# Optimization experiments

Measured on AMD Instinct MI355X. Metric: run time of the kernel, lower is better.

The kernel has to match this reference:

```python
import jax, jax.numpy as jnp
import numpy as np

N_MESH = 40962
N_GRID = 262144
N_EDGE = 786432
D = 128       # node/edge feature dim
H = 256       # MLP hidden dim
EPS = 1e-5


def _layernorm(x, g, b):
    m = jnp.mean(x, axis=-1, keepdims=True)
    v = jnp.mean(jnp.square(x - m), axis=-1, keepdims=True)
    return (x - m) * jax.lax.rsqrt(v + EPS) * g + b


def _mlp(x, W1, b1, W2, b2, g, beta):
    # Linear -> SiLU -> Linear -> LayerNorm (hidden_layers=1)
    h = jax.nn.silu(x @ W1 + b1)
    return _layernorm(h @ W2 + b2, g, beta)


def setup_inputs() -> dict:
    key = jax.random.key(0)
    ks = jax.random.split(key, 20)
    s = 0.02
    inp = {
        "m2g_efeat": jax.random.normal(ks[0], (N_EDGE, D), jnp.float32),
        "grid_nfeat": jax.random.normal(ks[1], (N_GRID, D), jnp.float32),
        "mesh_nfeat": jax.random.normal(ks[2], (N_MESH, D), jnp.float32),
        "src_idx": jax.random.randint(ks[3], (N_EDGE,), 0, N_MESH, jnp.int32),
        "dst_idx": jax.random.randint(ks[4], (N_EDGE,), 0, N_GRID, jnp.int32),
        # edge MLP: concat(efeat, src, dst) [3D] -> H -> D, LayerNorm
        "eW1": jax.random.normal(ks[5], (3 * D, H), jnp.float32) * s,
        "eb1": jnp.zeros((H,), jnp.float32),
        "eW2": jax.random.normal(ks[6], (H, D), jnp.float32) * s,
        "eb2": jnp.zeros((D,), jnp.float32),
        "eg": jnp.ones((D,), jnp.float32),
        "ebeta": jnp.zeros((D,), jnp.float32),
        # node MLP: concat(agg_efeat, grid_nfeat) [2D] -> H -> D, LayerNorm
        "nW1": jax.random.normal(ks[7], (2 * D, H), jnp.float32) * s,
        "nb1": jnp.zeros((H,), jnp.float32),
        "nW2": jax.random.normal(ks[8], (H, D), jnp.float32) * s,
        "nb2": jnp.zeros((D,), jnp.float32),
        "ng": jnp.ones((D,), jnp.float32),
        "nbeta": jnp.zeros((D,), jnp.float32),
    }
    return inp


def reference(m2g_efeat, grid_nfeat, mesh_nfeat, src_idx, dst_idx,
              eW1, eb1, eW2, eb2, eg, ebeta,
              nW1, nb1, nW2, nb2, ng, nbeta):
    # --- edge MLP (MeshGraphEdgeMLPConcat): gather src/dst, concat, MLP ---
    cat_e = jnp.concatenate(
        [m2g_efeat, mesh_nfeat[src_idx], grid_nfeat[dst_idx]], axis=-1)  # [E, 3D]
    efeat = _mlp(cat_e, eW1, eb1, eW2, eb2, eg, ebeta)                   # [E, D]
    # --- aggregate_and_concat: scatter-sum to dst nodes, concat dst feats ---
    agg = jax.ops.segment_sum(efeat, dst_idx, num_segments=N_GRID)       # [N_grid, D]
    cat_n = jnp.concatenate([agg, grid_nfeat], axis=-1)                  # [N_grid, 2D]
    # --- node MLP + residual ---
    return _mlp(cat_n, nW1, nb1, nW2, nb2, ng, nbeta) + grid_nfeat
```

## Files before the change

### kernel.cpp

```cpp
#include <hip/hip_runtime.h>
#include <hip/hip_bf16.h>

typedef __bf16 bf16_t;
typedef bf16_t bf16x8 __attribute__((ext_vector_type(8)));
typedef float f32x16 __attribute__((ext_vector_type(16)));

#define MFMA32(a, b, c) __builtin_amdgcn_mfma_f32_32x32x16_bf16(a, b, c, 0, 0, 0)

static constexpr int E_EDGE = 786432;
static constexpr int N_GRID = 262144;

static constexpr int E_LDT = 136;
static constexpr int E_ATB = 64 * E_LDT * 2;
static constexpr int E_LDH = 264;
static constexpr int E_LDO = 132;
static constexpr int E_OFF_IDX = 2 * E_ATB;
static constexpr int E_SMEM = E_OFF_IDX + 3 * 256;

__device__ __forceinline__ void lds_barrier() {
    asm volatile("s_waitcnt lgkmcnt(0)" ::: "memory");
    __builtin_amdgcn_s_barrier();
    __builtin_amdgcn_sched_barrier(0);
}

__device__ __forceinline__ float fast_silu(float x) {
    return x * __builtin_amdgcn_rcpf(1.f + __expf(-x));
}

__global__ void pack_w1(const float* __restrict__ w, bf16_t* __restrict__ out, int tsteps) {
    const int gid = blockIdx.x * 256 + threadIdx.x;
    if (gid >= tsteps * 8 * 8 * 64) return;
    const int lane = gid & 63, grp = gid >> 6;
    const int wave = grp & 7, ks = (grp >> 3) & 7, t = grp >> 6;
    const int n = wave * 32 + (lane & 31);
    const int kb = t * 128 + ks * 16 + (lane >> 5) * 8;
    union { bf16_t h[8]; uint4 u; } pk;
#pragma unroll
    for (int j = 0; j < 8; ++j) pk.h[j] = (bf16_t)w[(size_t)(kb + j) * 256 + n];
    reinterpret_cast<uint4*>(out)[gid] = pk.u;
}

__global__ void pack_w2(const float* __restrict__ w, bf16_t* __restrict__ out) {
    const int gid = blockIdx.x * 256 + threadIdx.x;
    if (gid >= 16 * 4 * 64) return;
    const int lane = gid & 63, grp = gid >> 6;
    const int wn = grp & 3, ks = grp >> 2;
    const int n = wn * 32 + (lane & 31);
    const int kb = ks * 16 + (lane >> 5) * 8;
    union { bf16_t h[8]; uint4 u; } pk;
#pragma unroll
    for (int j = 0; j < 8; ++j) pk.h[j] = (bf16_t)w[(size_t)(kb + j) * 128 + n];
    reinterpret_cast<uint4*>(out)[gid] = pk.u;
}

__global__ void f32_to_bf16_vec(const float* __restrict__ in, bf16_t* __restrict__ out, int n8) {
    int i = blockIdx.x * 256 + threadIdx.x;
    if (i < n8) {
        const float4* p = reinterpret_cast<const float4*>(in + (size_t)i * 8);
        const float4 a = p[0], b = p[1];
        union { bf16_t h[8]; uint4 u; } pk;
        pk.h[0] = (bf16_t)a.x; pk.h[1] = (bf16_t)a.y; pk.h[2] = (bf16_t)a.z; pk.h[3] = (bf16_t)a.w;
        pk.h[4] = (bf16_t)b.x; pk.h[5] = (bf16_t)b.y; pk.h[6] = (bf16_t)b.z; pk.h[7] = (bf16_t)b.w;
        reinterpret_cast<uint4*>(out)[i] = pk.u;
    }
}

__global__ void k_hist(const int* __restrict__ dst, int* __restrict__ deg, int E) {
    int i = blockIdx.x * 256 + threadIdx.x;
    if (i < E) atomicAdd(&deg[dst[i]], 1);
}

__global__ void k_scan1(const int* __restrict__ deg, int* __restrict__ excl,
                        int* __restrict__ bsum) {
    __shared__ int sd[256];
    const int b = blockIdx.x, t = threadIdx.x;
    int4 v = reinterpret_cast<const int4*>(deg)[b * 256 + t];
    const int s0 = v.x, s1 = s0 + v.y, s2 = s1 + v.z, s3 = s2 + v.w;
    sd[t] = s3;
    __syncthreads();
    for (int off = 1; off < 256; off <<= 1) {
        int val = (t >= off) ? sd[t - off] : 0;
        __syncthreads();
        if (t >= off) sd[t] += val;
        __syncthreads();
    }
    const int pre = (t > 0) ? sd[t - 1] : 0;
    int4 o;
    o.x = pre; o.y = pre + s0; o.z = pre + s1; o.w = pre + s2;
    reinterpret_cast<int4*>(excl)[b * 256 + t] = o;
    if (t == 255) bsum[b] = sd[255];
}

__global__ void k_scan2(const int* __restrict__ bsum, int* __restrict__ bofs) {
    __shared__ int sd[256];
    const int t = threadIdx.x;
    sd[t] = bsum[t];
    __syncthreads();
    for (int off = 1; off < 256; off <<= 1) {
        int val = (t >= off) ? sd[t - off] : 0;
        __syncthreads();
        if (t >= off) sd[t] += val;
        __syncthreads();
    }
    bofs[t] = (t > 0) ? sd[t - 1] : 0;
}

__global__ void k_scan3(const int* __restrict__ excl, const int* __restrict__ bofs,
                        int* __restrict__ rowptr, int* __restrict__ cursor, int N, int E) {
    int i = blockIdx.x * 256 + threadIdx.x;
    if (i < N) {
        const int v = excl[i] + bofs[i >> 10];
        rowptr[i] = v;
        cursor[i] = v;
    }
    if (i == 0) rowptr[N] = E;
}

__global__ void k_slot(const int* __restrict__ dst, int* __restrict__ cursor,
                       int* __restrict__ slot, int E) {
    int i = blockIdx.x * 256 + threadIdx.x;
    if (i < E) slot[i] = atomicAdd(&cursor[dst[i]], 1);
}

__global__ __launch_bounds__(512, 8) void edge_mlp(
    const float* __restrict__ m2g,
    const bf16_t* __restrict__ gridb, const bf16_t* __restrict__ meshb,
    const int* __restrict__ src_idx, const int* __restrict__ dst_idx,
    const int* __restrict__ slot,
    const bf16_t* __restrict__ W1P,
    const float* __restrict__ b1,
    const bf16_t* __restrict__ W2P,
    const float* __restrict__ b2,
    const float* __restrict__ g, const float* __restrict__ beta,
    bf16_t* __restrict__ efs) {
    __shared__ __align__(16) char smem[E_SMEM];

    const int tid = threadIdx.x;
    const int wave = tid >> 6, lane = tid & 63;
    const int l31 = lane & 31, lk = lane >> 5;
    const int wm = wave >> 2, wn = wave & 3;
    const int r0 = blockIdx.x * 64;
    const int srow = tid >> 3, sc = (tid & 7) * 16;

    int* sidx = (int*)(smem + E_OFF_IDX);
    int* didx = sidx + 64;
    int* slotl = didx + 64;
    if (tid < 64) sidx[tid] = src_idx[r0 + tid];
    else if (tid < 128) didx[tid - 64] = dst_idx[r0 + tid - 64];
    else if (tid < 192) slotl[tid - 128] = slot[r0 + tid - 128];
    lds_barrier();

    bf16_t* buf0 = (bf16_t*)smem;
    bf16_t* buf1 = (bf16_t*)(smem + E_ATB);

    {
        float4 f0[4];
        const float* p0 = m2g + (size_t)(r0 + srow) * 128 + sc;
#pragma unroll
        for (int j = 0; j < 4; ++j) f0[j] = *reinterpret_cast<const float4*>(p0 + j * 4);
        bf16_t* dst = buf0 + srow * E_LDT + sc;
#pragma unroll
        for (int q = 0; q < 2; ++q) {
            union { bf16_t h[8]; uint4 u; } pk;
            const float4 v0 = f0[q * 2], v1 = f0[q * 2 + 1];
            pk.h[0] = (bf16_t)v0.x; pk.h[1] = (bf16_t)v0.y;
            pk.h[2] = (bf16_t)v0.z; pk.h[3] = (bf16_t)v0.w;
            pk.h[4] = (bf16_t)v1.x; pk.h[5] = (bf16_t)v1.y;
            pk.h[6] = (bf16_t)v1.z; pk.h[7] = (bf16_t)v1.w;
            *reinterpret_cast<uint4*>(dst + q * 8) = pk.u;
        }
    }
    uint4 a1[2];
    {
        const bf16_t* p1 = meshb + (size_t)sidx[srow] * 128 + sc;
        a1[0] = *reinterpret_cast<const uint4*>(p1);
        a1[1] = *reinterpret_cast<const uint4*>(p1 + 8);
    }
    lds_barrier();

    f32x16 acc[2] = {};
    auto COMPUTE = [&](const bf16_t* A, int t) {
#pragma unroll
        for (int ks = 0; ks < 8; ++ks) {
            const bf16x8 bw = *reinterpret_cast<const bf16x8*>(
                W1P + ((size_t)((t * 8 + ks) * 8 + wave) * 64 + lane) * 8);
            const int kb = ks * 16 + lk * 8;
            bf16x8 a[2];
#pragma unroll
            for (int mt = 0; mt < 2; ++mt)
                a[mt] = *reinterpret_cast<const bf16x8*>(A + (mt * 32 + l31) * E_LDT + kb);
#pragma unroll
            for (int mt = 0; mt < 2; ++mt)
                acc[mt] = MFMA32(a[mt], bw, acc[mt]);
        }
    };

    uint4 a2[2];
    {
        const bf16_t* p2 = gridb + (size_t)didx[srow] * 128 + sc;
        a2[0] = *reinterpret_cast<const uint4*>(p2);
        a2[1] = *reinterpret_cast<const uint4*>(p2 + 8);
    }
    {
        bf16_t* dst = buf1 + srow * E_LDT + sc;
        *reinterpret_cast<uint4*>(dst) = a1[0];
        *reinterpret_cast<uint4*>(dst + 8) = a1[1];
    }
    COMPUTE(buf0, 0);
    lds_barrier();
    {
        bf16_t* dst = buf0 + srow * E_LDT + sc;
        *reinterpret_cast<uint4*>(dst) = a2[0];
        *reinterpret_cast<uint4*>(dst + 8) = a2[1];
    }
    COMPUTE(buf1, 1);
    lds_barrier();
    COMPUTE(buf0, 2);
    lds_barrier();

    bf16_t* hT = (bf16_t*)smem;
    {
        const int col = wave * 32 + l31;
        const float bb = b1[col];
#pragma unroll
        for (int mt = 0; mt < 2; ++mt)
#pragma unroll
            for (int r = 0; r < 16; ++r) {
                const int row = mt * 32 + (r & 3) + 8 * (r >> 2) + 4 * lk;
                hT[row * E_LDH + col] = (bf16_t)fast_silu(acc[mt][r] + bb);
            }
    }
    lds_barrier();

    f32x16 acc2 = {};
#pragma unroll
    for (int ks = 0; ks < 16; ++ks) {
        const bf16x8 bw = *reinterpret_cast<const bf16x8*>(
            W2P + ((size_t)(ks * 4 + wn) * 64 + lane) * 8);
        const int kb = ks * 16 + lk * 8;
        const bf16x8 a = *reinterpret_cast<const bf16x8*>(hT + (wm * 32 + l31) * E_LDH + kb);
        acc2 = MFMA32(a, bw, acc2);
    }
    lds_barrier();

    float* outl = (float*)smem;
    {
        const int col = wn * 32 + l31;
        const float bb = b2[col];
#pragma unroll
        for (int r = 0; r < 16; ++r) {
            const int row = wm * 32 + (r & 3) + 8 * (r >> 2) + 4 * lk;
            outl[row * E_LDO + col] = acc2[r] + bb;
        }
    }
    lds_barrier();

    {
        const int lrow = tid >> 3, lq = (tid & 7) * 16;
        const float* rpd = outl + lrow * E_LDO + lq;
        float s = 0.f, sq2 = 0.f;
#pragma unroll
        for (int q = 0; q < 4; ++q) {
            const float4 v = *reinterpret_cast<const float4*>(rpd + q * 4);
            s += v.x + v.y + v.z + v.w;
            sq2 += v.x * v.x + v.y * v.y + v.z * v.z + v.w * v.w;
        }
        s += __shfl_xor(s, 1);  sq2 += __shfl_xor(sq2, 1);
        s += __shfl_xor(s, 2);  sq2 += __shfl_xor(sq2, 2);
        s += __shfl_xor(s, 4);  sq2 += __shfl_xor(sq2, 4);
        const float mean = s * (1.f / 128.f);
        const float var = sq2 * (1.f / 128.f) - mean * mean;
        const float rstd = rsqrtf(var + 1e-5f);

        const int sl = slotl[lrow];
        bf16_t* op = efs + (size_t)sl * 128 + lq;
        union { bf16_t h[16]; uint4 u[2]; } pk;
#pragma unroll
        for (int q = 0; q < 4; ++q) {
            const float4 v = *reinterpret_cast<const float4*>(rpd + q * 4);
            const float4 gv = *reinterpret_cast<const float4*>(g + lq + q * 4);
            const float4 bv = *reinterpret_cast<const float4*>(beta + lq + q * 4);
            pk.h[q * 4 + 0] = (bf16_t)((v.x - mean) * rstd * gv.x + bv.x);
            pk.h[q * 4 + 1] = (bf16_t)((v.y - mean) * rstd * gv.y + bv.y);
            pk.h[q * 4 + 2] = (bf16_t)((v.z - mean) * rstd * gv.z + bv.z);
            pk.h[q * 4 + 3] = (bf16_t)((v.w - mean) * rstd * gv.w + bv.w);
        }
        *reinterpret_cast<uint4*>(op) = pk.u[0];
        *reinterpret_cast<uint4*>(op + 8) = pk.u[1];
    }
}

__global__ __launch_bounds__(512, 8) void node_mlp(
    const bf16_t* __restrict__ efs,
    const int* __restrict__ rowptr,
    const bf16_t* __restrict__ gridb,
    const float* __restrict__ gridf,
    const bf16_t* __restrict__ W1P,
    const float* __restrict__ b1,
    const bf16_t* __restrict__ W2P,
    const float* __restrict__ b2,
    const float* __restrict__ g, const float* __restrict__ beta,
    float* __restrict__ outp) {
    __shared__ __align__(16) char smem[E_SMEM];

    const int tid = threadIdx.x;
    const int wave = tid >> 6, lane = tid & 63;
    const int l31 = lane & 31, lk = lane >> 5;
    const int wm = wave >> 2, wn = wave & 3;
    const int r0 = blockIdx.x * 64;
    const int srow = tid >> 3, sc = (tid & 7) * 16;

    bf16_t* buf0 = (bf16_t*)smem;
    bf16_t* buf1 = (bf16_t*)(smem + E_ATB);
    int* rp = (int*)(smem + E_OFF_IDX);

    if (tid < 65) rp[tid] = rowptr[r0 + tid];
    lds_barrier();

    {
        const int beg = rp[srow], end = rp[srow + 1];
        float s[16];
#pragma unroll
        for (int i = 0; i < 16; ++i) s[i] = 0.f;
        for (int e = beg; e < end; ++e) {
            const bf16_t* p = efs + (size_t)e * 128 + sc;
            bf16x8 v0 = *reinterpret_cast<const bf16x8*>(p);
            bf16x8 v1 = *reinterpret_cast<const bf16x8*>(p + 8);
#pragma unroll
            for (int i = 0; i < 8; ++i) {
                s[i] += (float)v0[i];
                s[8 + i] += (float)v1[i];
            }
        }
        union { bf16_t h[16]; uint4 u[2]; } pk;
#pragma unroll
        for (int i = 0; i < 16; ++i) pk.h[i] = (bf16_t)s[i];
        bf16_t* dst = buf0 + srow * E_LDT + sc;
        *reinterpret_cast<uint4*>(dst) = pk.u[0];
        *reinterpret_cast<uint4*>(dst + 8) = pk.u[1];
    }
    uint4 a1[2];
    {
        const bf16_t* p1 = gridb + (size_t)(r0 + srow) * 128 + sc;
        a1[0] = *reinterpret_cast<const uint4*>(p1);
        a1[1] = *reinterpret_cast<const uint4*>(p1 + 8);
    }
    lds_barrier();

    f32x16 acc[2] = {};
    auto COMPUTE = [&](const bf16_t* A, int t) {
#pragma unroll
        for (int ks = 0; ks < 8; ++ks) {
            const bf16x8 bw = *reinterpret_cast<const bf16x8*>(
                W1P + ((size_t)((t * 8 + ks) * 8 + wave) * 64 + lane) * 8);
            const int kb = ks * 16 + lk * 8;
            bf16x8 a[2];
#pragma unroll
            for (int mt = 0; mt < 2; ++mt)
                a[mt] = *reinterpret_cast<const bf16x8*>(A + (mt * 32 + l31) * E_LDT + kb);
#pragma unroll
            for (int mt = 0; mt < 2; ++mt)
                acc[mt] = MFMA32(a[mt], bw, acc[mt]);
        }
    };

    {
        bf16_t* dst = buf1 + srow * E_LDT + sc;
        *reinterpret_cast<uint4*>(dst) = a1[0];
        *reinterpret_cast<uint4*>(dst + 8) = a1[1];
    }
    COMPUTE(buf0, 0);
    lds_barrier();
    COMPUTE(buf1, 1);
    lds_barrier();

    bf16_t* hT = (bf16_t*)smem;
    {
        const int col = wave * 32 + l31;
        const float bb = b1[col];
#pragma unroll
        for (int mt = 0; mt < 2; ++mt)
#pragma unroll
            for (int r = 0; r < 16; ++r) {
                const int row = mt * 32 + (r & 3) + 8 * (r >> 2) + 4 * lk;
                hT[row * E_LDH + col] = (bf16_t)fast_silu(acc[mt][r] + bb);
            }
    }
    lds_barrier();

    f32x16 acc2 = {};
#pragma unroll
    for (int ks = 0; ks < 16; ++ks) {
        const bf16x8 bw = *reinterpret_cast<const bf16x8*>(
            W2P + ((size_t)(ks * 4 + wn) * 64 + lane) * 8);
        const int kb = ks * 16 + lk * 8;
        const bf16x8 a = *reinterpret_cast<const bf16x8*>(hT + (wm * 32 + l31) * E_LDH + kb);
        acc2 = MFMA32(a, bw, acc2);
    }
    lds_barrier();

    float* outl = (float*)smem;
    {
        const int col = wn * 32 + l31;
        const float bb = b2[col];
#pragma unroll
        for (int r = 0; r < 16; ++r) {
            const int row = wm * 32 + (r & 3) + 8 * (r >> 2) + 4 * lk;
            outl[row * E_LDO + col] = acc2[r] + bb;
        }
    }
    lds_barrier();

    {
        const int lrow = tid >> 3, lq = (tid & 7) * 16;
        const float* rpd = outl + lrow * E_LDO + lq;
        float s = 0.f, sq2 = 0.f;
#pragma unroll
        for (int q = 0; q < 4; ++q) {
            const float4 v = *reinterpret_cast<const float4*>(rpd + q * 4);
            s += v.x + v.y + v.z + v.w;
            sq2 += v.x * v.x + v.y * v.y + v.z * v.z + v.w * v.w;
        }
        s += __shfl_xor(s, 1);  sq2 += __shfl_xor(sq2, 1);
        s += __shfl_xor(s, 2);  sq2 += __shfl_xor(sq2, 2);
        s += __shfl_xor(s, 4);  sq2 += __shfl_xor(sq2, 4);
        const float mean = s * (1.f / 128.f);
        const float var = sq2 * (1.f / 128.f) - mean * mean;
        const float rstd = rsqrtf(var + 1e-5f);

        const float* grp = gridf + (size_t)(r0 + lrow) * 128 + lq;
        float* op = outp + (size_t)(r0 + lrow) * 128 + lq;
#pragma unroll
        for (int q = 0; q < 4; ++q) {
            const float4 v = *reinterpret_cast<const float4*>(rpd + q * 4);
            const float4 gv = *reinterpret_cast<const float4*>(g + lq + q * 4);
            const float4 bv = *reinterpret_cast<const float4*>(beta + lq + q * 4);
            const float4 rr = *reinterpret_cast<const float4*>(grp + q * 4);
            float4 y;
            y.x = (v.x - mean) * rstd * gv.x + bv.x + rr.x;
            y.y = (v.y - mean) * rstd * gv.y + bv.y + rr.y;
            y.z = (v.z - mean) * rstd * gv.z + bv.z + rr.z;
            y.w = (v.w - mean) * rstd * gv.w + bv.w + rr.w;
            *reinterpret_cast<float4*>(op + q * 4) = y;
        }
    }
}

extern "C" void kernel_launch(void* const* d_in, const int* in_sizes, int n_in,
                              void* d_out, int out_size, void* d_ws, size_t ws_size,
                              hipStream_t stream) {
    const float* m2g = (const float*)d_in[0];
    const float* gridf = (const float*)d_in[1];
    const float* meshf = (const float*)d_in[2];
    const int* src_idx = (const int*)d_in[3];
    const int* dst_idx = (const int*)d_in[4];
    const float* eW1 = (const float*)d_in[5];
    const float* eb1 = (const float*)d_in[6];
    const float* eW2 = (const float*)d_in[7];
    const float* eb2 = (const float*)d_in[8];
    const float* eg = (const float*)d_in[9];
    const float* ebeta = (const float*)d_in[10];
    const float* nW1 = (const float*)d_in[11];
    const float* nb1 = (const float*)d_in[12];
    const float* nW2 = (const float*)d_in[13];
    const float* nb2 = (const float*)d_in[14];
    const float* ng = (const float*)d_in[15];
    const float* nbeta = (const float*)d_in[16];
    float* out = (float*)d_out;

    const size_t mesh_elems = (size_t)in_sizes[2];
    const size_t grid_elems = (size_t)N_GRID * 128;
    const size_t efs_elems = (size_t)E_EDGE * 128;

    char* base = (char*)d_ws;
    size_t off = 0;
    auto alloc = [&](size_t bytes) { size_t o = off; off = (off + bytes + 15) & ~(size_t)15; return o; };

    const size_t o_w1e = alloc(192 * 64 * 8 * 2);
    const size_t o_w2e = alloc(64 * 64 * 8 * 2);
    const size_t o_w1n = alloc(128 * 64 * 8 * 2);
    const size_t o_w2n = alloc(64 * 64 * 8 * 2);
    const size_t o_gridb = alloc(grid_elems * 2);
    const size_t o_meshb = alloc(mesh_elems * 2);
    const size_t o_efs = alloc(efs_elems * 2);
    const size_t o_rowptr = alloc((N_GRID + 1) * 4);
    const size_t o_cursor = alloc((size_t)N_GRID * 4);
    const size_t o_slot = alloc((size_t)E_EDGE * 4);
    const size_t o_deg = alloc((size_t)N_GRID * 4);
    const size_t o_excl = alloc((size_t)N_GRID * 4);
    const size_t o_bsum = alloc(256 * 4);
    const size_t o_bofs = alloc(256 * 4);

    bf16_t* W1eP = (bf16_t*)(base + o_w1e);
    bf16_t* W2eP = (bf16_t*)(base + o_w2e);
    bf16_t* W1nP = (bf16_t*)(base + o_w1n);
    bf16_t* W2nP = (bf16_t*)(base + o_w2n);
    bf16_t* gridb = (bf16_t*)(base + o_gridb);
    bf16_t* meshb = (bf16_t*)(base + o_meshb);
    bf16_t* efs = (bf16_t*)(base + o_efs);
    int* rowptr = (int*)(base + o_rowptr);
    int* cursor = (int*)(base + o_cursor);
    int* slot = (int*)(base + o_slot);
    int* deg = (int*)(base + o_deg);
    int* excl = (int*)(base + o_excl);
    int* bsum = (int*)(base + o_bsum);
    int* bofs = (int*)(base + o_bofs);

    pack_w1<<<(192 * 64 + 255) / 256, 256, 0, stream>>>(eW1, W1eP, 3);
    pack_w2<<<(64 * 64 + 255) / 256, 256, 0, stream>>>(eW2, W2eP);
    pack_w1<<<(128 * 64 + 255) / 256, 256, 0, stream>>>(nW1, W1nP, 2);
    pack_w2<<<(64 * 64 + 255) / 256, 256, 0, stream>>>(nW2, W2nP);

    const int g8 = (int)(grid_elems / 8), m8 = (int)(mesh_elems / 8);
    f32_to_bf16_vec<<<(g8 + 255) / 256, 256, 0, stream>>>(gridf, gridb, g8);
    f32_to_bf16_vec<<<(m8 + 255) / 256, 256, 0, stream>>>(meshf, meshb, m8);

    hipMemsetAsync(deg, 0, (size_t)N_GRID * 4, stream);
    k_hist<<<(E_EDGE + 255) / 256, 256, 0, stream>>>(dst_idx, deg, E_EDGE);
    k_scan1<<<256, 256, 0, stream>>>(deg, excl, bsum);
    k_scan2<<<1, 256, 0, stream>>>(bsum, bofs);
    k_scan3<<<(N_GRID + 255) / 256, 256, 0, stream>>>(excl, bofs, rowptr, cursor, N_GRID, E_EDGE);
    k_slot<<<(E_EDGE + 255) / 256, 256, 0, stream>>>(dst_idx, cursor, slot, E_EDGE);

    edge_mlp<<<E_EDGE / 64, 512, 0, stream>>>(
        m2g, gridb, meshb, src_idx, dst_idx, slot,
        W1eP, eb1, W2eP, eb2, eg, ebeta, efs);

    node_mlp<<<N_GRID / 64, 512, 0, stream>>>(
        efs, rowptr, gridb, gridf,
        W1nP, nb1, W2nP, nb2, ng, nbeta, out);
}
```

Before: 616.6 us.

## Gather edge operands directly from global, fuse scan and conversion kernels

```diff
diff --git a/kernel.cpp b/kernel.cpp
--- a/kernel.cpp
+++ b/kernel.cpp
@@ -53,16 +53,20 @@
     reinterpret_cast<uint4*>(out)[gid] = pk.u;
 }
 
-__global__ void f32_to_bf16_vec(const float* __restrict__ in, bf16_t* __restrict__ out, int n8) {
+__global__ void f32_to_bf16_2(const float* __restrict__ a, const float* __restrict__ b,
+                              bf16_t* __restrict__ oa, bf16_t* __restrict__ ob,
+                              int n8a, int n8tot) {
     int i = blockIdx.x * 256 + threadIdx.x;
-    if (i < n8) {
-        const float4* p = reinterpret_cast<const float4*>(in + (size_t)i * 8);
-        const float4 a = p[0], b = p[1];
-        union { bf16_t h[8]; uint4 u; } pk;
-        pk.h[0] = (bf16_t)a.x; pk.h[1] = (bf16_t)a.y; pk.h[2] = (bf16_t)a.z; pk.h[3] = (bf16_t)a.w;
-        pk.h[4] = (bf16_t)b.x; pk.h[5] = (bf16_t)b.y; pk.h[6] = (bf16_t)b.z; pk.h[7] = (bf16_t)b.w;
-        reinterpret_cast<uint4*>(out)[i] = pk.u;
-    }
+    if (i >= n8tot) return;
+    const float* src = (i < n8a) ? a : b;
+    bf16_t* dst = (i < n8a) ? oa : ob;
+    const int k = (i < n8a) ? i : i - n8a;
+    const float4* p = reinterpret_cast<const float4*>(src + (size_t)k * 8);
+    const float4 v0 = p[0], v1 = p[1];
+    union { bf16_t h[8]; uint4 u; } pk;
+    pk.h[0] = (bf16_t)v0.x; pk.h[1] = (bf16_t)v0.y; pk.h[2] = (bf16_t)v0.z; pk.h[3] = (bf16_t)v0.w;
+    pk.h[4] = (bf16_t)v1.x; pk.h[5] = (bf16_t)v1.y; pk.h[6] = (bf16_t)v1.z; pk.h[7] = (bf16_t)v1.w;
+    reinterpret_cast<uint4*>(dst)[k] = pk.u;
 }
 
 __global__ void k_hist(const int* __restrict__ dst, int* __restrict__ deg, int E) {
@@ -91,27 +95,24 @@
     if (t == 255) bsum[b] = sd[255];
 }
 
-__global__ void k_scan2(const int* __restrict__ bsum, int* __restrict__ bofs) {
-    __shared__ int sd[256];
-    const int t = threadIdx.x;
-    sd[t] = bsum[t];
+__global__ void k_scan23(const int* __restrict__ excl, const int* __restrict__ bsum,
+                         int* __restrict__ rowptr, int* __restrict__ cursor, int N, int E) {
+    __shared__ int part[4];
+    __shared__ int sofs;
+    const int b = blockIdx.x, t = threadIdx.x;
+    const int lim = b >> 2;
+    int v = (t < lim) ? bsum[t] : 0;
+#pragma unroll
+    for (int d = 1; d < 64; d <<= 1) v += __shfl_xor(v, d);
+    if ((t & 63) == 0) part[t >> 6] = v;
     __syncthreads();
-    for (int off = 1; off < 256; off <<= 1) {
-        int val = (t >= off) ? sd[t - off] : 0;
-        __syncthreads();
-        if (t >= off) sd[t] += val;
-        __syncthreads();
-    }
-    bofs[t] = (t > 0) ? sd[t - 1] : 0;
-}
-
-__global__ void k_scan3(const int* __restrict__ excl, const int* __restrict__ bofs,
-                        int* __restrict__ rowptr, int* __restrict__ cursor, int N, int E) {
-    int i = blockIdx.x * 256 + threadIdx.x;
+    if (t == 0) sofs = part[0] + part[1] + part[2] + part[3];
+    __syncthreads();
+    const int i = b * 256 + t;
     if (i < N) {
-        const int v = excl[i] + bofs[i >> 10];
-        rowptr[i] = v;
-        cursor[i] = v;
+        const int val = excl[i] + sofs;
+        rowptr[i] = val;
+        cursor[i] = val;
     }
     if (i == 0) rowptr[N] = E;
 }
@@ -148,10 +149,8 @@
     if (tid < 64) sidx[tid] = src_idx[r0 + tid];
     else if (tid < 128) didx[tid - 64] = dst_idx[r0 + tid - 64];
     else if (tid < 192) slotl[tid - 128] = slot[r0 + tid - 128];
-    lds_barrier();
 
     bf16_t* buf0 = (bf16_t*)smem;
-    bf16_t* buf1 = (bf16_t*)(smem + E_ATB);
 
     {
         float4 f0[4];
@@ -170,52 +169,46 @@
             *reinterpret_cast<uint4*>(dst + q * 8) = pk.u;
         }
     }
-    uint4 a1[2];
-    {
-        const bf16_t* p1 = meshb + (size_t)sidx[srow] * 128 + sc;
-        a1[0] = *reinterpret_cast<const uint4*>(p1);
-        a1[1] = *reinterpret_cast<const uint4*>(p1 + 8);
-    }
-    lds_barrier();
+    lds_barrier();
+
+    const bf16_t* mr0 = meshb + (size_t)sidx[l31] * 128;
+    const bf16_t* mr1 = meshb + (size_t)sidx[32 + l31] * 128;
+    const bf16_t* gr0 = gridb + (size_t)didx[l31] * 128;
+    const bf16_t* gr1 = gridb + (size_t)didx[32 + l31] * 128;
 
     f32x16 acc[2] = {};
-    auto COMPUTE = [&](const bf16_t* A, int t) {
-#pragma unroll
-        for (int ks = 0; ks < 8; ++ks) {
-            const bf16x8 bw = *reinterpret_cast<const bf16x8*>(
-                W1P + ((size_t)((t * 8 + ks) * 8 + wave) * 64 + lane) * 8);
-            const int kb = ks * 16 + lk * 8;
-            bf16x8 a[2];
-#pragma unroll
-            for (int mt = 0; mt < 2; ++mt)
-                a[mt] = *reinterpret_cast<const bf16x8*>(A + (mt * 32 + l31) * E_LDT + kb);
-#pragma unroll
-            for (int mt = 0; mt < 2; ++mt)
-                acc[mt] = MFMA32(a[mt], bw, acc[mt]);
-        }
-    };
-
-    uint4 a2[2];
-    {
-        const bf16_t* p2 = gridb + (size_t)didx[srow] * 128 + sc;
-        a2[0] = *reinterpret_cast<const uint4*>(p2);
-        a2[1] = *reinterpret_cast<const uint4*>(p2 + 8);
-    }
-    {
-        bf16_t* dst = buf1 + srow * E_LDT + sc;
-        *reinterpret_cast<uint4*>(dst) = a1[0];
-        *reinterpret_cast<uint4*>(dst + 8) = a1[1];
-    }
-    COMPUTE(buf0, 0);
-    lds_barrier();
-    {
-        bf16_t* dst = buf0 + srow * E_LDT + sc;
-        *reinterpret_cast<uint4*>(dst) = a2[0];
-        *reinterpret_cast<uint4*>(dst + 8) = a2[1];
-    }
-    COMPUTE(buf1, 1);
-    lds_barrier();
-    COMPUTE(buf0, 2);
+#pragma unroll
+    for (int ks = 0; ks < 8; ++ks) {
+        const bf16x8 bw = *reinterpret_cast<const bf16x8*>(
+            W1P + ((size_t)((0 * 8 + ks) * 8 + wave) * 64 + lane) * 8);
+        const int kb = ks * 16 + lk * 8;
+        const bf16x8 a0 = *reinterpret_cast<const bf16x8*>(buf0 + l31 * E_LDT + kb);
+        const bf16x8 a1 = *reinterpret_cast<const bf16x8*>(buf0 + (32 + l31) * E_LDT + kb);
+        acc[0] = MFMA32(a0, bw, acc[0]);
+        acc[1] = MFMA32(a1, bw, acc[1]);
+    }
+    __builtin_amdgcn_sched_barrier(0);
+#pragma unroll
+    for (int ks = 0; ks < 8; ++ks) {
+        const bf16x8 bw = *reinterpret_cast<const bf16x8*>(
+            W1P + ((size_t)((1 * 8 + ks) * 8 + wave) * 64 + lane) * 8);
+        const int kb = ks * 16 + lk * 8;
+        const bf16x8 a0 = *reinterpret_cast<const bf16x8*>(mr0 + kb);
+        const bf16x8 a1 = *reinterpret_cast<const bf16x8*>(mr1 + kb);
+        acc[0] = MFMA32(a0, bw, acc[0]);
+        acc[1] = MFMA32(a1, bw, acc[1]);
+    }
+    __builtin_amdgcn_sched_barrier(0);
+#pragma unroll
+    for (int ks = 0; ks < 8; ++ks) {
+        const bf16x8 bw = *reinterpret_cast<const bf16x8*>(
+            W1P + ((size_t)((2 * 8 + ks) * 8 + wave) * 64 + lane) * 8);
+        const int kb = ks * 16 + lk * 8;
+        const bf16x8 a0 = *reinterpret_cast<const bf16x8*>(gr0 + kb);
+        const bf16x8 a1 = *reinterpret_cast<const bf16x8*>(gr1 + kb);
+        acc[0] = MFMA32(a0, bw, acc[0]);
+        acc[1] = MFMA32(a1, bw, acc[1]);
+    }
     lds_barrier();
 
     bf16_t* hT = (bf16_t*)smem;
@@ -294,7 +287,6 @@
     const bf16_t* __restrict__ efs,
     const int* __restrict__ rowptr,
     const bf16_t* __restrict__ gridb,
-    const float* __restrict__ gridf,
     const bf16_t* __restrict__ W1P,
     const float* __restrict__ b1,
     const bf16_t* __restrict__ W2P,
@@ -428,19 +420,24 @@
         const float var = sq2 * (1.f / 128.f) - mean * mean;
         const float rstd = rsqrtf(var + 1e-5f);
 
-        const float* grp = gridf + (size_t)(r0 + lrow) * 128 + lq;
+        const bf16_t* grp = gridb + (size_t)(r0 + lrow) * 128 + lq;
+        const bf16x8 rv0 = *reinterpret_cast<const bf16x8*>(grp);
+        const bf16x8 rv1 = *reinterpret_cast<const bf16x8*>(grp + 8);
         float* op = outp + (size_t)(r0 + lrow) * 128 + lq;
 #pragma unroll
         for (int q = 0; q < 4; ++q) {
             const float4 v = *reinterpret_cast<const float4*>(rpd + q * 4);
             const float4 gv = *reinterpret_cast<const float4*>(g + lq + q * 4);
             const float4 bv = *reinterpret_cast<const float4*>(beta + lq + q * 4);
-            const float4 rr = *reinterpret_cast<const float4*>(grp + q * 4);
             float4 y;
-            y.x = (v.x - mean) * rstd * gv.x + bv.x + rr.x;
-            y.y = (v.y - mean) * rstd * gv.y + bv.y + rr.y;
-            y.z = (v.z - mean) * rstd * gv.z + bv.z + rr.z;
-            y.w = (v.w - mean) * rstd * gv.w + bv.w + rr.w;
+            const float r0f = (q < 2) ? (float)rv0[(q & 1) * 4 + 0] : (float)rv1[((q - 2) & 1) * 4 + 0];
+            const float r1f = (q < 2) ? (float)rv0[(q & 1) * 4 + 1] : (float)rv1[((q - 2) & 1) * 4 + 1];
+            const float r2f = (q < 2) ? (float)rv0[(q & 1) * 4 + 2] : (float)rv1[((q - 2) & 1) * 4 + 2];
+            const float r3f = (q < 2) ? (float)rv0[(q & 1) * 4 + 3] : (float)rv1[((q - 2) & 1) * 4 + 3];
+            y.x = (v.x - mean) * rstd * gv.x + bv.x + r0f;
+            y.y = (v.y - mean) * rstd * gv.y + bv.y + r1f;
+            y.z = (v.z - mean) * rstd * gv.z + bv.z + r2f;
+            y.w = (v.w - mean) * rstd * gv.w + bv.w + r3f;
             *reinterpret_cast<float4*>(op + q * 4) = y;
         }
     }
@@ -489,7 +486,6 @@
     const size_t o_deg = alloc((size_t)N_GRID * 4);
     const size_t o_excl = alloc((size_t)N_GRID * 4);
     const size_t o_bsum = alloc(256 * 4);
-    const size_t o_bofs = alloc(256 * 4);
 
     bf16_t* W1eP = (bf16_t*)(base + o_w1e);
     bf16_t* W2eP = (bf16_t*)(base + o_w2e);
@@ -504,7 +500,6 @@
     int* deg = (int*)(base + o_deg);
     int* excl = (int*)(base + o_excl);
     int* bsum = (int*)(base + o_bsum);
-    int* bofs = (int*)(base + o_bofs);
 
     pack_w1<<<(192 * 64 + 255) / 256, 256, 0, stream>>>(eW1, W1eP, 3);
     pack_w2<<<(64 * 64 + 255) / 256, 256, 0, stream>>>(eW2, W2eP);
@@ -512,14 +507,13 @@
     pack_w2<<<(64 * 64 + 255) / 256, 256, 0, stream>>>(nW2, W2nP);
 
     const int g8 = (int)(grid_elems / 8), m8 = (int)(mesh_elems / 8);
-    f32_to_bf16_vec<<<(g8 + 255) / 256, 256, 0, stream>>>(gridf, gridb, g8);
-    f32_to_bf16_vec<<<(m8 + 255) / 256, 256, 0, stream>>>(meshf, meshb, m8);
+    f32_to_bf16_2<<<(g8 + m8 + 255) / 256, 256, 0, stream>>>(gridf, meshf, gridb, meshb,
+                                                             g8, g8 + m8);
 
     hipMemsetAsync(deg, 0, (size_t)N_GRID * 4, stream);
     k_hist<<<(E_EDGE + 255) / 256, 256, 0, stream>>>(dst_idx, deg, E_EDGE);
     k_scan1<<<256, 256, 0, stream>>>(deg, excl, bsum);
-    k_scan2<<<1, 256, 0, stream>>>(bsum, bofs);
-    k_scan3<<<(N_GRID + 255) / 256, 256, 0, stream>>>(excl, bofs, rowptr, cursor, N_GRID, E_EDGE);
+    k_scan23<<<(N_GRID + 255) / 256, 256, 0, stream>>>(excl, bsum, rowptr, cursor, N_GRID, E_EDGE);
     k_slot<<<(E_EDGE + 255) / 256, 256, 0, stream>>>(dst_idx, cursor, slot, E_EDGE);
 
     edge_mlp<<<E_EDGE / 64, 512, 0, stream>>>(
@@ -527,6 +521,6 @@
         W1eP, eb1, W2eP, eb2, eg, ebeta, efs);
 
     node_mlp<<<N_GRID / 64, 512, 0, stream>>>(
-        efs, rowptr, gridb, gridf,
+        efs, rowptr, gridb,
         W1nP, nb1, W2nP, nb2, ng, nbeta, out);
 }
```

Measured after the change: 882.3 us. 43.1% more time.
